# Performance work log

Measured on AMD Instinct MI355X. Metric: run time of the kernel, lower is better.

Reference implementation:

```python
import jax, jax.numpy as jnp
import numpy as np

PAD_VALUE = -1e10  # matches torch F.pad(value=-1e10); padded cells are sliced away before output


def setup_inputs() -> dict:
    key = jax.random.key(0)
    x = jax.random.normal(key, (8, 16, 256, 256), dtype=jnp.float32)
    return {"x": x, "d": 5}


def reference(x, d):
    # x: (B, C, H, W). Builds a shift-graph: each pixel connects to the d*d-1
    # pixels in a d x d window; weight = -||f1-f2||^2 * sqrt(di^2+dj^2).
    B, C, H, W = x.shape
    r = d // 2
    id0 = jnp.arange(H * W, dtype=jnp.int32).reshape(H, W)
    img_pad = jnp.pad(x, ((0, 0), (0, 0), (r, r), (r, r)), constant_values=PAD_VALUE)
    ws, edges = [], []
    for i in range(d):
        for j in range(d):
            if i == r and j == r:
                continue
            pos_v = (i - r) * W + (j - r)
            # shifted view of the padded image, aligned with x: (B, C, H, W)
            f1 = img_pad[:, :, i:H + i, j:W + j]
            scale = float(((i - r) ** 2 + (j - r) ** 2) ** 0.5)
            dist = -((f1 - x) ** 2).sum(axis=1) * scale  # (B, H, W)
            # crop to the region where the shifted neighbor is in-bounds
            h0, h1 = max(r - i, 0), H - max(i - r, 0)
            w0, w1 = max(r - j, 0), W - max(j - r, 0)
            imgx = dist[:, h0:h1, w0:w1].reshape(B, -1)  # (B, n_ij)
            idx = id0[h0:h1, w0:w1].reshape(-1)          # (n_ij,)
            pos = jnp.broadcast_to(idx[None, :], (B, idx.shape[0]))
            ws.append(imgx)
            edges.append(jnp.stack((pos, pos + pos_v), axis=-1))  # (B, n_ij, 2)
    return jnp.concatenate(edges, axis=-2), jnp.concatenate(ws, axis=-1)
```

## Files before the change

kernel.cpp:

```cpp
#include <hip/hip_runtime.h>


#define HH 256
#define WW 256
#define CC 16
#define BB 8
#define HW (HH * WW)
#define EE 1557540

__global__ __launch_bounds__(256) void shiftgraph_kernel(
    const float* __restrict__ x, float* __restrict__ out) {
    __shared__ float lds[3080];
    const int bid = blockIdx.x;
    const int b = bid & 7;
    const int h = bid >> 3;
    const int w = threadIdx.x;

    const float* __restrict__ xb = x + (size_t)b * (CC * HW);

    const float* src[3];
    int dst[3];
#pragma unroll
    for (int inst = 0; inst < 3; ++inst) {
        const int flatf = inst * 1024 + w * 4;
        const int cl  = flatf / 768;
        const int rem = flatf - cl * 768;
        const int row = rem >> 8;
        const int col = rem & 255;
        int hr = h + row; hr = hr > HH - 1 ? HH - 1 : hr;
        src[inst] = xb + cl * HW + hr * WW + col;
        dst[inst] = flatf;
    }

    float acc[12];
#pragma unroll
    for (int s2 = 0; s2 < 12; ++s2) acc[s2] = 0.0f;

    for (int cc = 0; cc < 4; ++cc) {
        __syncthreads();
#pragma unroll
        for (int inst = 0; inst < 3; ++inst) {
            const float4 v = *reinterpret_cast<const float4*>(src[inst]);
            *reinterpret_cast<float4*>(&lds[dst[inst]]) = v;
            src[inst] += 4 * HW;
        }
        __syncthreads();
#pragma unroll
        for (int c = 0; c < 4; ++c) {
            const int base = c * 768 + w;
            const float ctr = lds[base];
            float d;
            d = lds[base + 1] - ctr; acc[0] = fmaf(d, d, acc[0]);
            d = lds[base + 2] - ctr; acc[1] = fmaf(d, d, acc[1]);
#pragma unroll
            for (int dj = -2; dj <= 2; ++dj) {
                d = lds[base + 256 + dj] - ctr;
                acc[4 + dj] = fmaf(d, d, acc[4 + dj]);
                d = lds[base + 512 + dj] - ctr;
                acc[9 + dj] = fmaf(d, d, acc[9 + dj]);
            }
        }
    }

    float* __restrict__ edges = out;
    float* __restrict__ wsp   = out + (size_t)BB * EE * 2;
    const size_t bE = (size_t)b * EE;
    const int posc = h * WW + w;

    int s = 0;
#pragma unroll
    for (int di = 0; di <= 2; ++di) {
#pragma unroll
        for (int dj = (di == 0 ? 1 : -2); dj <= 2; ++dj, ++s) {
            const int i = di + 2, j = dj + 2;
            if (h + di >= HH) continue;
            const int w2 = w + dj;
            if (w2 < 0 || w2 >= WW) continue;

            const float scale = sqrtf((float)(di * di + dj * dj));
            const float wsv = -acc[s] * scale;

            int offF = 0, offM = 0;
#pragma unroll
            for (int m = 0; m < 25; ++m) {
                const int mi = m / 5, mj = m % 5;
                if (mi == 2 && mj == 2) continue;
                const int cm = (HH - (mi < 2 ? 2 - mi : mi - 2)) *
                               (WW - (mj < 2 ? 2 - mj : mj - 2));
                if (m < i * 5 + j) offF += cm;
                if (m < (4 - i) * 5 + (4 - j)) offM += cm;
            }
            const int cww = WW - (dj < 0 ? -dj : dj);
            const int e1 = offF + h * cww + (w - (dj < 0 ? -dj : 0));
            const int e2 = offM + h * cww + (w + (dj < 0 ? dj : 0));
            const int posv = di * WW + dj;

            union { float f[2]; unsigned long long u; } evF, evM;
            evF.f[0] = (float)posc;          evF.f[1] = (float)(posc + posv);
            evM.f[0] = (float)(posc + posv); evM.f[1] = (float)posc;

            __builtin_nontemporal_store(
                evF.u, reinterpret_cast<unsigned long long*>(edges + (bE + e1) * 2));
            __builtin_nontemporal_store(
                evM.u, reinterpret_cast<unsigned long long*>(edges + (bE + e2) * 2));
            __builtin_nontemporal_store(wsv, wsp + bE + e1);
            __builtin_nontemporal_store(wsv, wsp + bE + e2);
        }
    }
}

extern "C" void kernel_launch(void* const* d_in, const int* in_sizes, int n_in,
                              void* d_out, int out_size, void* d_ws, size_t ws_size,
                              hipStream_t stream) {
    const float* x = (const float*)d_in[0];
    float* out = (float*)d_out;
    dim3 block(WW);
    dim3 grid(HH * BB);
    shiftgraph_kernel<<<grid, block, 0, stream>>>(x, out);
}
```

Measured before the change: 35.39 us.

## Process two output rows per block and double-buffer channel loads in LDS

Each block now handles two image rows with 512 threads, so the loaded halo of four rows serves two outputs instead of three rows serving one. This cuts the redundant global reads of x. Channel chunks are double-buffered in LDS, with the next chunk prefetched into registers while the current one is computed, which removes one barrier per iteration. The cost is more LDS per block and fewer blocks, which may lower occupancy. The kernel is likely dominated by output writes, so the gain may be small.

```diff
diff --git a/kernel.cpp b/kernel.cpp
--- a/kernel.cpp
+++ b/kernel.cpp
@@ -8,57 +8,74 @@
 #define HW (HH * WW)
 #define EE 1557540
 
-__global__ __launch_bounds__(256) void shiftgraph_kernel(
+__global__ __launch_bounds__(512) void shiftgraph_kernel(
     const float* __restrict__ x, float* __restrict__ out) {
-    __shared__ float lds[3080];
+    __shared__ float lds[2][4096];
     const int bid = blockIdx.x;
-    const int b = bid & 7;
-    const int h = bid >> 3;
-    const int w = threadIdx.x;
+    const int b  = bid & 7;
+    const int hg = bid >> 3;
+    const int tid = threadIdx.x;
+    const int rr = tid >> 8;
+    const int w  = tid & 255;
+    const int h  = hg * 2 + rr;
 
     const float* __restrict__ xb = x + (size_t)b * (CC * HW);
 
-    const float* src[3];
-    int dst[3];
+    const float* src[2];
+    int dst[2];
 #pragma unroll
-    for (int inst = 0; inst < 3; ++inst) {
-        const int flatf = inst * 1024 + w * 4;
-        const int cl  = flatf / 768;
-        const int rem = flatf - cl * 768;
+    for (int inst = 0; inst < 2; ++inst) {
+        const int flatf = inst * 2048 + tid * 4;
+        const int cl  = flatf >> 10;
+        const int rem = flatf & 1023;
         const int row = rem >> 8;
         const int col = rem & 255;
-        int hr = h + row; hr = hr > HH - 1 ? HH - 1 : hr;
+        int hr = hg * 2 + row; hr = hr > HH - 1 ? HH - 1 : hr;
         src[inst] = xb + cl * HW + hr * WW + col;
         dst[inst] = flatf;
     }
+
+#pragma unroll
+    for (int inst = 0; inst < 2; ++inst) {
+        const float4 v = *reinterpret_cast<const float4*>(src[inst]);
+        *reinterpret_cast<float4*>(&lds[0][dst[inst]]) = v;
+        src[inst] += 4 * HW;
+    }
+    __syncthreads();
 
     float acc[12];
 #pragma unroll
     for (int s2 = 0; s2 < 12; ++s2) acc[s2] = 0.0f;
 
+#pragma unroll
     for (int cc = 0; cc < 4; ++cc) {
-        __syncthreads();
-#pragma unroll
-        for (int inst = 0; inst < 3; ++inst) {
-            const float4 v = *reinterpret_cast<const float4*>(src[inst]);
-            *reinterpret_cast<float4*>(&lds[dst[inst]]) = v;
-            src[inst] += 4 * HW;
+        float4 nv0, nv1;
+        if (cc < 3) {
+            nv0 = *reinterpret_cast<const float4*>(src[0]);
+            nv1 = *reinterpret_cast<const float4*>(src[1]);
+            src[0] += 4 * HW; src[1] += 4 * HW;
         }
-        __syncthreads();
+        const float* __restrict__ buf = lds[cc & 1];
 #pragma unroll
         for (int c = 0; c < 4; ++c) {
-            const int base = c * 768 + w;
-            const float ctr = lds[base];
+            const int base = c * 1024 + rr * 256 + w;
+            const float ctr = buf[base];
             float d;
-            d = lds[base + 1] - ctr; acc[0] = fmaf(d, d, acc[0]);
-            d = lds[base + 2] - ctr; acc[1] = fmaf(d, d, acc[1]);
+            d = buf[base + 1] - ctr; acc[0] = fmaf(d, d, acc[0]);
+            d = buf[base + 2] - ctr; acc[1] = fmaf(d, d, acc[1]);
 #pragma unroll
             for (int dj = -2; dj <= 2; ++dj) {
-                d = lds[base + 256 + dj] - ctr;
+                d = buf[base + 256 + dj] - ctr;
                 acc[4 + dj] = fmaf(d, d, acc[4 + dj]);
-                d = lds[base + 512 + dj] - ctr;
+                d = buf[base + 512 + dj] - ctr;
                 acc[9 + dj] = fmaf(d, d, acc[9 + dj]);
             }
+        }
+        if (cc < 3) {
+            float* __restrict__ nb = lds[(cc + 1) & 1];
+            *reinterpret_cast<float4*>(&nb[dst[0]]) = nv0;
+            *reinterpret_cast<float4*>(&nb[dst[1]]) = nv1;
+            __syncthreads();
         }
     }
 
@@ -114,7 +131,7 @@
                               hipStream_t stream) {
     const float* x = (const float*)d_in[0];
     float* out = (float*)d_out;
-    dim3 block(WW);
-    dim3 grid(HH * BB);
+    dim3 block(512);
+    dim3 grid(128 * BB);
     shiftgraph_kernel<<<grid, block, 0, stream>>>(x, out);
 }
```

Result: no change. 35.94 us (+1.5%).
